# Optimization experiments

Measured on AMD Instinct MI355X. Metric: run time of the kernel, lower is better.

Reference implementation:

```python
import jax, jax.numpy as jnp
import numpy as np

K = 8192  # num_embeddings
D = 512   # embedding_dim
BETA = 0.25


def setup_inputs() -> dict:
    key = jax.random.key(0)
    k1, k2, k3 = jax.random.split(key, 3)
    B, T = 64, 512
    latents = jax.random.normal(k1, (B, T, D), dtype=jnp.float32)
    # nn.Embedding weight initialized uniform(-1/K, 1/K)
    emb = jax.random.uniform(k2, (K, D), dtype=jnp.float32, minval=-1.0 / K, maxval=1.0 / K)
    gold_encoding_inds = jax.random.randint(k3, (B * T, 1), 0, K, dtype=jnp.int64 if jax.config.jax_enable_x64 else jnp.int32)
    return {"gold_encoding_inds": gold_encoding_inds, "latents": latents, "epc": 1, "emb": emb}


def reference(gold_encoding_inds, latents, epc, emb):
    B, T, _ = latents.shape
    flat = latents.reshape(B * T, D)  # [N, D]
    # squared euclidean distance to every codebook entry: [N, K]
    dist = (jnp.sum(flat * flat, axis=1, keepdims=True)
            + jnp.sum(emb * emb, axis=1)
            - 2.0 * jnp.matmul(flat, emb.T))
    encoding_inds = jnp.argmin(dist, axis=1)[:, None]  # [N, 1]
    # one-hot @ emb  ==  gather rows of emb
    quantized = emb[encoding_inds[:, 0]].reshape(B, T, D)
    # per-position MSE over the feature dim
    commitment_loss = jnp.mean((jax.lax.stop_gradient(quantized) - latents) ** 2, axis=-1)
    embedding_loss = jnp.mean((quantized - jax.lax.stop_gradient(latents)) ** 2, axis=-1)
    vq_loss = embedding_loss + BETA * commitment_loss  # [B, T]
    # straight-through estimator
    quantized = latents + jax.lax.stop_gradient(quantized - latents)
    correct = jnp.sum(gold_encoding_inds == encoding_inds)
    total = jnp.asarray(gold_encoding_inds.shape[0], dtype=jnp.int32)
    return quantized, vq_loss, encoding_inds.T, (correct, total)
```

## Files before the change

kernel.cpp:

```cpp
#include <hip/hip_runtime.h>
#include <math.h>

#define N_ROWS 32768
#define KCB    8192
#define DIM    512
#define BETA   0.25f
#define MARGIN 2e-3f
#define FLAG_SLACK 1e-4f
#define CAND_CAP 256

typedef __attribute__((ext_vector_type(4))) float  f32x4;
typedef __attribute__((ext_vector_type(4))) int    i32x4;
typedef __attribute__((ext_vector_type(8))) int    i32x8;

__device__ __forceinline__ unsigned short f2h(float x) {
    _Float16 h = (_Float16)x;
    return *(unsigned short*)&h;
}
__device__ __forceinline__ float h2f(unsigned short u) {
    _Float16 h = *(_Float16*)&u;
    return (float)h;
}

#define SQ_BLOCKS ((N_ROWS + KCB) / 8)
__global__ __launch_bounds__(256) void pre_kernel(
        const float* __restrict__ lat, const float* __restrict__ emb,
        float* __restrict__ row_sq, float* __restrict__ emb_sq,
        unsigned char* __restrict__ latq, unsigned char* __restrict__ embq,
        int* __restrict__ counter) {
    if (blockIdx.x < SQ_BLOCKS) {
#pragma clang fp contract(off)
        if (blockIdx.x == 0 && threadIdx.x == 0) *counter = 0;
        const int w    = threadIdx.x >> 6;
        const int lane = threadIdx.x & 63;
        const int half = lane >> 5;
        const int L    = lane & 31;
        const int b    = L >> 3, j = L & 7;
        const int row  = blockIdx.x * 8 + w * 2 + half;
        const float* p = (row < N_ROWS) ? (lat + (size_t)row * DIM)
                                        : (emb + (size_t)(row - N_ROWS) * DIM);
        const float* q = p + 128 * b + j;
        float a0 = q[0];
        float r  = a0 * a0;
        for (int i = 1; i < 16; ++i) {
            float a = q[8 * i];
            float s = a * a;
            r = r + s;
        }
        r = r + __shfl_xor(r, 1);
        r = r + __shfl_xor(r, 2);
        r = r + __shfl_xor(r, 4);
        r = r + __shfl_xor(r, 8);
        r = r + __shfl_xor(r, 16);
        if (L == 0) {
            if (row < N_ROWS) row_sq[row] = r;
            else              emb_sq[row - N_ROWS] = r;
        }
    } else {
        const size_t NL8 = (size_t)N_ROWS * DIM / 8;
        const size_t NE8 = (size_t)KCB * DIM / 8;
        size_t g = (size_t)(blockIdx.x - SQ_BLOCKS) * 256 + threadIdx.x;
        const float* src; unsigned char* dst; size_t i; float sc;
        if (g < NL8)            { src = lat; dst = latq; i = g;       sc = 1.0f; }
        else if (g < NL8 + NE8) { src = emb; dst = embq; i = g - NL8; sc = 8192.0f; }
        else return;
        float4 v0 = ((const float4*)src)[2 * i];
        float4 v1 = ((const float4*)src)[2 * i + 1];
        int lo = __builtin_amdgcn_cvt_pk_fp8_f32(v0.x * sc, v0.y * sc, 0,  false);
        lo     = __builtin_amdgcn_cvt_pk_fp8_f32(v0.z * sc, v0.w * sc, lo, true);
        int hi = __builtin_amdgcn_cvt_pk_fp8_f32(v1.x * sc, v1.y * sc, 0,  false);
        hi     = __builtin_amdgcn_cvt_pk_fp8_f32(v1.z * sc, v1.w * sc, hi, true);
        ((int2*)dst)[i] = make_int2(lo, hi);
    }
}

__device__ __forceinline__ void load16_to_lds(const void* g, void* l) {
    __builtin_amdgcn_global_load_lds(
        (const __attribute__((address_space(1))) unsigned int*)g,
        (__attribute__((address_space(3))) unsigned int*)l, 16, 0, 0);
}

__global__ __launch_bounds__(256, 2) void gemm_kernel(
        const unsigned char* __restrict__ latq,
        const unsigned char* __restrict__ embq,
        const float* __restrict__ emb_sq,
        unsigned int* __restrict__ packed) {
    __shared__ unsigned char Ac[2][128 * 128];
    __shared__ unsigned char Br[2][128 * 128];

    const int tid   = threadIdx.x;
    const int w     = tid >> 6;
    const int lane  = tid & 63;
    const int q     = lane >> 4;
    const int m16   = lane & 15;

    const int b   = blockIdx.x;
    const int l   = (b & 7) * 2048 + (b >> 3);
    const int st  = l >> 9;
    const int r2  = l & 511;
    const int rg  = st & 7;
    const int cg  = st >> 3;
    const int row0  = (rg * 32 + (r2 & 31)) * 128;
    const int code0 = (cg * 16 + (r2 >> 5)) * 128;

    const int wc    = 64 * (w >> 1);
    const int rbase = 64 * (w & 1);

    int soff[8];
#pragma unroll
    for (int i = 0; i < 8; ++i) {
        int cid   = w * 8 + i;
        int h     = cid & 15;
        int base0 = (cid < 16) ? code0 : row0;
        soff[i] = (base0 + h * 8 + (lane >> 3)) * DIM
                + (((lane & 7) ^ (lane >> 3)) << 4);
    }

#define STAGE(bsel, k0)                                                     \
    do {                                                                    \
        _Pragma("unroll")                                                   \
        for (int i = 0; i < 8; ++i) {                                       \
            int cid = w * 8 + i;                                            \
            const unsigned char* g =                                        \
                ((cid < 16) ? embq : latq) + soff[i] + (k0);                \
            unsigned char* dst = ((cid < 16) ? &Ac[bsel][0] : &Br[bsel][0]) \
                               + (cid & 15) * 1024;                         \
            load16_to_lds(g, dst);                                          \
        }                                                                   \
    } while (0)

    f32x4 acc[4][4];
#pragma unroll
    for (int r = 0; r < 4; ++r)
#pragma unroll
        for (int c = 0; c < 4; ++c) acc[r][c] = (f32x4){0.f, 0.f, 0.f, 0.f};

    const int sw = (m16 & 7) << 4;

    STAGE(0, 0);

#pragma unroll
    for (int t = 0; t < 4; ++t) {
        const int bsel = t & 1;
        if (t < 3) STAGE((t + 1) & 1, (t + 1) * 128);
        __builtin_amdgcn_sched_barrier(0);
        if (t < 3) { asm volatile("s_waitcnt vmcnt(8)" ::: "memory"); }
        else       { asm volatile("s_waitcnt vmcnt(0)" ::: "memory"); }
        __builtin_amdgcn_s_barrier();
        __builtin_amdgcn_sched_barrier(0);

        i32x8 af[4];
#pragma unroll
        for (int r = 0; r < 4; ++r) {
            int roff = (wc + 16 * r + m16) * 128;
            i32x4 lo = *(const i32x4*)&Ac[bsel][roff + ((q * 32) ^ sw)];
            i32x4 hi = *(const i32x4*)&Ac[bsel][roff + ((q * 32 + 16) ^ sw)];
            af[r] = (i32x8){lo[0], lo[1], lo[2], lo[3],
                            hi[0], hi[1], hi[2], hi[3]};
        }
#pragma unroll
        for (int c = 0; c < 4; ++c) {
            int roff = (rbase + 16 * c + m16) * 128;
            i32x4 lo = *(const i32x4*)&Br[bsel][roff + ((q * 32) ^ sw)];
            i32x4 hi = *(const i32x4*)&Br[bsel][roff + ((q * 32 + 16) ^ sw)];
            i32x8 bv = (i32x8){lo[0], lo[1], lo[2], lo[3],
                               hi[0], hi[1], hi[2], hi[3]};
#pragma unroll
            for (int r = 0; r < 4; ++r)
                acc[r][c] = __builtin_amdgcn_mfma_scale_f32_16x16x128_f8f6f4(
                    af[r], bv, acc[r][c],
                    0, 0,
                    0, 0x7F7F7F7F,
                    0, 0x7F7F7F7F);
        }
        __builtin_amdgcn_sched_barrier(0);
        __builtin_amdgcn_s_barrier();
        __builtin_amdgcn_sched_barrier(0);
    }
#undef STAGE

    float sev[4][4];
#pragma unroll
    for (int r = 0; r < 4; ++r)
#pragma unroll
        for (int reg = 0; reg < 4; ++reg)
            sev[r][reg] = emb_sq[code0 + wc + 16 * r + 4 * q + reg];

    const float inv = 1.0f / 4096.0f;
#pragma unroll
    for (int c = 0; c < 4; ++c) {
        unsigned pk[4];
#pragma unroll
        for (int r = 0; r < 4; ++r) {
            float s0 = sev[r][0] - acc[r][c][0] * inv;
            float s1 = sev[r][1] - acc[r][c][1] * inv;
            float s2 = sev[r][2] - acc[r][c][2] * inv;
            float s3 = sev[r][3] - acc[r][c][3] * inv;
            float mn = fminf(fminf(s0, s1), fminf(s2, s3));
            mn = fminf(mn, __shfl_xor(mn, 16));
            mn = fminf(mn, __shfl_xor(mn, 32));
            float t = mn + MARGIN;
            unsigned nib = (s0 <= t ? 1u : 0u) | (s1 <= t ? 2u : 0u)
                         | (s2 <= t ? 4u : 0u) | (s3 <= t ? 8u : 0u);
            nib <<= (4 * q);
            nib |= (unsigned)__shfl_xor((int)nib, 16);
            nib |= (unsigned)__shfl_xor((int)nib, 32);
            pk[r] = ((unsigned)f2h(mn)) | (nib << 16);
        }
        if (lane < 16) {
            int grow = row0 + rbase + 16 * c + m16;
            int base = (code0 + wc) >> 4;
            *(uint4*)&packed[(size_t)grow * 512 + base] =
                make_uint4(pk[0], pk[1], pk[2], pk[3]);
        }
    }
}

__global__ __launch_bounds__(256) void argmin_out_kernel(
        const float* __restrict__ lat, const float* __restrict__ emb,
        const float* __restrict__ row_sq, const float* __restrict__ emb_sq,
        const unsigned int* __restrict__ packed,
        const int* __restrict__ gold,
        float* __restrict__ out, int* __restrict__ counter) {
    __shared__ float xs[4][DIM];
    __shared__ int   s_cnt[4];
    __shared__ int   s_list[4][CAND_CAP];
    const int w    = threadIdx.x >> 6;
    const int lane = threadIdx.x & 63;
    const int row  = blockIdx.x * 4 + w;

    {
        const float4* xp = (const float4*)(lat + (size_t)row * DIM);
        ((float4*)xs[w])[lane]      = xp[lane];
        ((float4*)xs[w])[lane + 64] = xp[lane + 64];
    }
    const float sx = row_sq[row];
    const float* xw = xs[w];

    unsigned u[8];
    {
        const uint4* tb = (const uint4*)(packed + (size_t)row * 512 + lane * 8);
        uint4 v0 = tb[0], v1 = tb[1];
        u[0] = v0.x; u[1] = v0.y; u[2] = v0.z; u[3] = v0.w;
        u[4] = v1.x; u[5] = v1.y; u[6] = v1.z; u[7] = v1.w;
    }
    float tm[8];
#pragma unroll
    for (int j = 0; j < 8; ++j) tm[j] = h2f((unsigned short)(u[j] & 0xFFFFu));
    float m = tm[0];
#pragma unroll
    for (int j = 1; j < 8; ++j) m = fminf(m, tm[j]);
#pragma unroll
    for (int off = 1; off < 64; off <<= 1)
        m = fminf(m, __shfl_xor(m, off));
    const float thresh = m + (MARGIN + FLAG_SLACK);

    if (lane == 0) s_cnt[w] = 0;
    __syncthreads();
#pragma unroll
    for (int j = 0; j < 8; ++j) {
        if (tm[j] <= thresh) {
            int g = lane * 8 + j;
            unsigned bm = u[j] >> 16;
            while (bm) {
                int b = __ffs(bm) - 1;
                bm &= bm - 1;
                int pos = atomicAdd(&s_cnt[w], 1);
                if (pos < CAND_CAP) s_list[w][pos] = g * 16 + b;
            }
        }
    }
    __syncthreads();
    const int cnt = min(s_cnt[w], CAND_CAP);

    float bd = INFINITY;
    int   bi = 0x7fffffff;
    for (int base = 0; base < cnt; base += 64) {
        int ci = base + lane;
        float dvl = INFINITY;
        int   cl  = 0x7fffffff;
        if (ci < cnt) {
            int code = s_list[w][ci];
            const float* ep = emb + (size_t)code * DIM;
            float acc = 0.0f;
            for (int d = 0; d < DIM; d += 8) {
                float ev[8], xv[8];
#pragma unroll
                for (int t = 0; t < 8; ++t) { ev[t] = ep[d + t]; xv[t] = xw[d + t]; }
#pragma unroll
                for (int t = 0; t < 8; ++t) acc = fmaf(xv[t], ev[t], acc);
            }
            float a = sx + emb_sq[code];
            dvl = a - 2.0f * acc;
            cl  = code;
        }
        if (dvl < bd || (dvl == bd && cl < bi)) { bd = dvl; bi = cl; }
    }
#pragma unroll
    for (int off = 1; off < 64; off <<= 1) {
        float od = __shfl_xor(bd, off);
        int   oi = __shfl_xor(bi, off);
        if (od < bd || (od == bd && oi < bi)) { bd = od; bi = oi; }
    }
    const int idx = bi;

    const float4* e4 = (const float4*)(emb + (size_t)idx * DIM);
    float4*       q4 = (float4*)(out + (size_t)row * DIM);
    q4[lane]      = e4[lane];
    q4[lane + 64] = e4[lane + 64];

    float r = 0.0f;
    if (lane < 32) {
        const int b = lane >> 3, j = lane & 7;
        const float* ep = emb + (size_t)idx * DIM + b * 128 + j;
        const float* xp = xw + b * 128 + j;
        for (int i = 0; i < 16; ++i) {
            float dq = ep[8 * i] - xp[8 * i];
            float s  = dq * dq;
            r = (i == 0) ? s : (r + s);
        }
    }
    for (int mm = 1; mm <= 16; mm <<= 1) {
        float o = __shfl_xor(r, mm);
        r = r + o;
    }
    if (lane == 0) {
        float mean = r * (1.0f / 512.0f);
        float v    = mean + 0.25f * mean;
        out[(size_t)N_ROWS * DIM + row]          = v;
        out[(size_t)N_ROWS * DIM + N_ROWS + row] = (float)idx;
        if (gold[row] == idx) atomicAdd(counter, 1);
    }
}

__global__ void tail_kernel(const int* __restrict__ counter,
                            float* __restrict__ out) {
    if (threadIdx.x == 0 && blockIdx.x == 0) {
        const size_t off = (size_t)N_ROWS * DIM + 2 * (size_t)N_ROWS;
        out[off]     = (float)(*counter);
        out[off + 1] = (float)N_ROWS;
    }
}

__global__ __launch_bounds__(256) void sq_kernel(
        const float* __restrict__ lat, const float* __restrict__ emb,
        float* __restrict__ row_sq, float* __restrict__ emb_sq) {
#pragma clang fp contract(off)
    const int w    = threadIdx.x >> 6;
    const int lane = threadIdx.x & 63;
    const int half = lane >> 5;
    const int L    = lane & 31;
    const int b    = L >> 3, j = L & 7;
    const int row  = blockIdx.x * 8 + w * 2 + half;
    if (row >= N_ROWS + KCB) return;
    const float* p = (row < N_ROWS) ? (lat + (size_t)row * DIM)
                                    : (emb + (size_t)(row - N_ROWS) * DIM);
    const float* q = p + 128 * b + j;
    float a0 = q[0];
    float r  = a0 * a0;
    for (int i = 1; i < 16; ++i) {
        float a = q[8 * i];
        float s = a * a;
        r = r + s;
    }
    r = r + __shfl_xor(r, 1);
    r = r + __shfl_xor(r, 2);
    r = r + __shfl_xor(r, 4);
    r = r + __shfl_xor(r, 8);
    r = r + __shfl_xor(r, 16);
    if (L == 0) {
        if (row < N_ROWS) row_sq[row] = r;
        else              emb_sq[row - N_ROWS] = r;
    }
}

#define BM 64
#define BK 128
#define BD 32
__global__ __launch_bounds__(256) void dist_kernel(
        const float* __restrict__ lat, const float* __restrict__ emb,
        const float* __restrict__ row_sq, const float* __restrict__ emb_sq,
        int* __restrict__ enc) {
    __shared__ float xsh[BD][BM];
    __shared__ float esh[BD][BK];
    const int tid  = threadIdx.x;
    const int trow = tid >> 4;
    const int tcol = tid & 15;
    const int row0 = blockIdx.x * BM;
    float bd[4]; int bi[4];
    for (int i = 0; i < 4; ++i) { bd[i] = INFINITY; bi[i] = 0; }
    float sx[4];
    for (int i = 0; i < 4; ++i) sx[i] = row_sq[row0 + 4 * trow + i];
    for (int kt = 0; kt < KCB; kt += BK) {
        float acc[4][8] = {};
        for (int d0 = 0; d0 < DIM; d0 += BD) {
            for (int f = tid; f < BM * BD / 4; f += 256) {
                int r = f >> 3, c4 = f & 7;
                float4 v = *(const float4*)(lat + (size_t)(row0 + r) * DIM + d0 + 4 * c4);
                xsh[4 * c4 + 0][r] = v.x; xsh[4 * c4 + 1][r] = v.y;
                xsh[4 * c4 + 2][r] = v.z; xsh[4 * c4 + 3][r] = v.w;
            }
            for (int f = tid; f < BK * BD / 4; f += 256) {
                int r = f >> 3, c4 = f & 7;
                float4 v = *(const float4*)(emb + (size_t)(kt + r) * DIM + d0 + 4 * c4);
                esh[4 * c4 + 0][r] = v.x; esh[4 * c4 + 1][r] = v.y;
                esh[4 * c4 + 2][r] = v.z; esh[4 * c4 + 3][r] = v.w;
            }
            __syncthreads();
            for (int dd = 0; dd < BD; ++dd) {
                float4 xv  = *(const float4*)&xsh[dd][4 * trow];
                float4 ev0 = *(const float4*)&esh[dd][8 * tcol];
                float4 ev1 = *(const float4*)&esh[dd][8 * tcol + 4];
                float xr[4] = { xv.x, xv.y, xv.z, xv.w };
                float ec[8] = { ev0.x, ev0.y, ev0.z, ev0.w, ev1.x, ev1.y, ev1.z, ev1.w };
                for (int r = 0; r < 4; ++r)
                    for (int c = 0; c < 8; ++c)
                        acc[r][c] = fmaf(xr[r], ec[c], acc[r][c]);
            }
            __syncthreads();
        }
        for (int c = 0; c < 8; ++c) {
            int   code = kt + 8 * tcol + c;
            float se   = emb_sq[code];
            for (int r = 0; r < 4; ++r) {
                float a  = sx[r] + se;
                float dv = a - 2.0f * acc[r][c];
                if (dv < bd[r]) { bd[r] = dv; bi[r] = code; }
            }
        }
    }
    for (int off = 1; off < 16; off <<= 1) {
        for (int r = 0; r < 4; ++r) {
            float od = __shfl_xor(bd[r], off);
            int   oi = __shfl_xor(bi[r], off);
            if (od < bd[r] || (od == bd[r] && oi < bi[r])) { bd[r] = od; bi[r] = oi; }
        }
    }
    if (tcol == 0)
        for (int r = 0; r < 4; ++r)
            enc[row0 + 4 * trow + r] = bi[r];
}

__global__ void out_kernel(const float* __restrict__ lat,
                           const float* __restrict__ emb,
                           const int* __restrict__ gold,
                           const int* __restrict__ enc,
                           float* __restrict__ out,
                           int* __restrict__ counter) {
#pragma clang fp contract(off)
    const int gid  = blockIdx.x * blockDim.x + threadIdx.x;
    const int row  = gid >> 6;
    const int lane = threadIdx.x & 63;
    if (row >= N_ROWS) return;
    const int idx = enc[row];
    const float4* e4 = (const float4*)(emb + (size_t)idx * DIM);
    float4*       q4 = (float4*)(out + (size_t)row * DIM);
    q4[lane]      = e4[lane];
    q4[lane + 64] = e4[lane + 64];
    float r = 0.0f;
    if (lane < 32) {
        const int b = lane >> 3, j = lane & 7;
        const float* ep = emb + (size_t)idx * DIM + b * 128 + j;
        const float* xp = lat + (size_t)row * DIM + b * 128 + j;
        for (int i = 0; i < 16; ++i) {
            float dq = ep[8 * i] - xp[8 * i];
            float s  = dq * dq;
            r = (i == 0) ? s : (r + s);
        }
    }
    for (int m = 1; m <= 16; m <<= 1) {
        float o = __shfl_xor(r, m);
        r = r + o;
    }
    if (lane == 0) {
        float mean = r * (1.0f / 512.0f);
        float v    = mean + 0.25f * mean;
        out[(size_t)N_ROWS * DIM + row]          = v;
        out[(size_t)N_ROWS * DIM + N_ROWS + row] = (float)idx;
        if (gold[row] == idx) atomicAdd(counter, 1);
    }
}

extern "C" void kernel_launch(void* const* d_in, const int* in_sizes, int n_in,
                              void* d_out, int out_size, void* d_ws, size_t ws_size,
                              hipStream_t stream) {
    (void)in_sizes; (void)n_in; (void)out_size;
    const int*   gold = (const int*)d_in[0];
    const float* lat  = (const float*)d_in[1];
    const float* emb  = (const float*)d_in[3];
    float* out = (float*)d_out;

    const size_t SZ_LATQ = (size_t)N_ROWS * DIM;
    const size_t SZ_EMBQ = (size_t)KCB * DIM;
    const size_t SZ_PK   = (size_t)N_ROWS * 512 * 4;
    const size_t SZ_SMALL = (size_t)N_ROWS * 4 + (size_t)KCB * 4 + 256;
    const size_t NEEDED = SZ_LATQ + SZ_EMBQ + SZ_PK + SZ_SMALL;

    if (ws_size >= NEEDED) {
        unsigned char* w8 = (unsigned char*)d_ws;
        unsigned char* latq    = w8;
        unsigned char* embq    = w8 + SZ_LATQ;
        unsigned int*  packed  = (unsigned int*)(w8 + SZ_LATQ + SZ_EMBQ);
        float*         row_sq  = (float*)(w8 + SZ_LATQ + SZ_EMBQ + SZ_PK);
        float*         emb_sq  = row_sq + N_ROWS;
        int*           counter = (int*)(emb_sq + KCB);

        const int pre_blocks = SQ_BLOCKS + (N_ROWS + KCB) * (DIM / 8) / 256;
        pre_kernel<<<pre_blocks, 256, 0, stream>>>(
            lat, emb, row_sq, emb_sq, latq, embq, counter);
        gemm_kernel<<<(N_ROWS / 128) * (KCB / 128), 256, 0, stream>>>(
            latq, embq, emb_sq, packed);
        argmin_out_kernel<<<N_ROWS / 4, 256, 0, stream>>>(
            lat, emb, row_sq, emb_sq, packed, gold, out, counter);
        tail_kernel<<<1, 64, 0, stream>>>(counter, out);
    } else {
        float* row_sq  = (float*)d_ws;
        float* emb_sq  = row_sq + N_ROWS;
        int*   enc     = (int*)(emb_sq + KCB);
        int*   counter = enc + N_ROWS;
        hipMemsetAsync(counter, 0, sizeof(int), stream);
        sq_kernel<<<(N_ROWS + KCB) / 8, 256, 0, stream>>>(lat, emb, row_sq, emb_sq);
        dist_kernel<<<N_ROWS / BM, 256, 0, stream>>>(lat, emb, row_sq, emb_sq, enc);
        out_kernel<<<N_ROWS / 4, 256, 0, stream>>>(lat, emb, gold, enc, out, counter);
        tail_kernel<<<1, 64, 0, stream>>>(counter, out);
    }
}
```

Baseline: 538.8 us.

## Enlarge GEMM tile to 256x256 with 512 threads and XCD-aware block mapping

```diff
diff --git a/kernel.cpp b/kernel.cpp
--- a/kernel.cpp
+++ b/kernel.cpp
@@ -80,38 +80,38 @@
         (__attribute__((address_space(3))) unsigned int*)l, 16, 0, 0);
 }
 
-__global__ __launch_bounds__(256, 2) void gemm_kernel(
+__global__ __launch_bounds__(512, 2) void gemm_kernel(
         const unsigned char* __restrict__ latq,
         const unsigned char* __restrict__ embq,
         const float* __restrict__ emb_sq,
         unsigned int* __restrict__ packed) {
-    __shared__ unsigned char Ac[2][128 * 128];
-    __shared__ unsigned char Br[2][128 * 128];
-
-    const int tid   = threadIdx.x;
-    const int w     = tid >> 6;
-    const int lane  = tid & 63;
-    const int q     = lane >> 4;
-    const int m16   = lane & 15;
+    __shared__ unsigned char Ac[2][256 * 128];
+    __shared__ unsigned char Br[2][256 * 128];
+
+    const int tid  = threadIdx.x;
+    const int w    = tid >> 6;
+    const int lane = tid & 63;
+    const int q    = lane >> 4;
+    const int m16  = lane & 15;
 
     const int b   = blockIdx.x;
-    const int l   = (b & 7) * 2048 + (b >> 3);
-    const int st  = l >> 9;
-    const int r2  = l & 511;
-    const int rg  = st & 7;
-    const int cg  = st >> 3;
-    const int row0  = (rg * 32 + (r2 & 31)) * 128;
-    const int code0 = (cg * 16 + (r2 >> 5)) * 128;
-
-    const int wc    = 64 * (w >> 1);
-    const int rbase = 64 * (w & 1);
+    const int xcd = b & 7;
+    const int id  = b >> 3;
+    const int st  = id >> 6;
+    const int rw  = id & 15;
+    const int cw  = (id >> 4) & 3;
+    const int row0  = (st * 16 + rw) * 256;
+    const int code0 = (xcd * 4 + cw) * 256;
+
+    const int wc2 = (w & 1) * 128;
+    const int wr  = (w >> 1) * 64;
 
     int soff[8];
 #pragma unroll
     for (int i = 0; i < 8; ++i) {
         int cid   = w * 8 + i;
-        int h     = cid & 15;
-        int base0 = (cid < 16) ? code0 : row0;
+        int h     = cid & 31;
+        int base0 = (cid < 32) ? code0 : row0;
         soff[i] = (base0 + h * 8 + (lane >> 3)) * DIM
                 + (((lane & 7) ^ (lane >> 3)) << 4);
     }
@@ -122,18 +122,18 @@
         for (int i = 0; i < 8; ++i) {                                       \
             int cid = w * 8 + i;                                            \
             const unsigned char* g =                                        \
-                ((cid < 16) ? embq : latq) + soff[i] + (k0);                \
-            unsigned char* dst = ((cid < 16) ? &Ac[bsel][0] : &Br[bsel][0]) \
-                               + (cid & 15) * 1024;                         \
+                ((cid < 32) ? embq : latq) + soff[i] + (k0);                \
+            unsigned char* dst = ((cid < 32) ? &Ac[bsel][0] : &Br[bsel][0]) \
+                               + (cid & 31) * 1024;                         \
             load16_to_lds(g, dst);                                          \
         }                                                                   \
     } while (0)
 
-    f32x4 acc[4][4];
-#pragma unroll
-    for (int r = 0; r < 4; ++r)
-#pragma unroll
-        for (int c = 0; c < 4; ++c) acc[r][c] = (f32x4){0.f, 0.f, 0.f, 0.f};
+    f32x4 acc[8][4];
+#pragma unroll
+    for (int g = 0; g < 8; ++g)
+#pragma unroll
+        for (int c = 0; c < 4; ++c) acc[g][c] = (f32x4){0.f, 0.f, 0.f, 0.f};
 
     const int sw = (m16 & 7) << 4;
 
@@ -149,29 +149,38 @@
         __builtin_amdgcn_s_barrier();
         __builtin_amdgcn_sched_barrier(0);
 
-        i32x8 af[4];
-#pragma unroll
-        for (int r = 0; r < 4; ++r) {
-            int roff = (wc + 16 * r + m16) * 128;
-            i32x4 lo = *(const i32x4*)&Ac[bsel][roff + ((q * 32) ^ sw)];
-            i32x4 hi = *(const i32x4*)&Ac[bsel][roff + ((q * 32 + 16) ^ sw)];
-            af[r] = (i32x8){lo[0], lo[1], lo[2], lo[3],
-                            hi[0], hi[1], hi[2], hi[3]};
-        }
+        i32x8 bv[4];
 #pragma unroll
         for (int c = 0; c < 4; ++c) {
-            int roff = (rbase + 16 * c + m16) * 128;
+            int roff = (wr + 16 * c + m16) * 128;
             i32x4 lo = *(const i32x4*)&Br[bsel][roff + ((q * 32) ^ sw)];
             i32x4 hi = *(const i32x4*)&Br[bsel][roff + ((q * 32 + 16) ^ sw)];
-            i32x8 bv = (i32x8){lo[0], lo[1], lo[2], lo[3],
-                               hi[0], hi[1], hi[2], hi[3]};
-#pragma unroll
-            for (int r = 0; r < 4; ++r)
-                acc[r][c] = __builtin_amdgcn_mfma_scale_f32_16x16x128_f8f6f4(
-                    af[r], bv, acc[r][c],
-                    0, 0,
-                    0, 0x7F7F7F7F,
-                    0, 0x7F7F7F7F);
+            bv[c] = (i32x8){lo[0], lo[1], lo[2], lo[3],
+                            hi[0], hi[1], hi[2], hi[3]};
+        }
+#pragma unroll
+        for (int hh = 0; hh < 2; ++hh) {
+            i32x8 af[4];
+#pragma unroll
+            for (int g = 0; g < 4; ++g) {
+                int roff = (wc2 + 16 * (hh * 4 + g) + m16) * 128;
+                i32x4 lo = *(const i32x4*)&Ac[bsel][roff + ((q * 32) ^ sw)];
+                i32x4 hi = *(const i32x4*)&Ac[bsel][roff + ((q * 32 + 16) ^ sw)];
+                af[g] = (i32x8){lo[0], lo[1], lo[2], lo[3],
+                                hi[0], hi[1], hi[2], hi[3]};
+            }
+            __builtin_amdgcn_s_setprio(1);
+#pragma unroll
+            for (int g = 0; g < 4; ++g)
+#pragma unroll
+                for (int c = 0; c < 4; ++c)
+                    acc[hh * 4 + g][c] =
+                        __builtin_amdgcn_mfma_scale_f32_16x16x128_f8f6f4(
+                            af[g], bv[c], acc[hh * 4 + g][c],
+                            0, 0,
+                            0, 0x7F7F7F7F,
+                            0, 0x7F7F7F7F);
+            __builtin_amdgcn_s_setprio(0);
         }
         __builtin_amdgcn_sched_barrier(0);
         __builtin_amdgcn_s_barrier();
@@ -179,23 +188,23 @@
     }
 #undef STAGE
 
-    float sev[4][4];
-#pragma unroll
-    for (int r = 0; r < 4; ++r)
-#pragma unroll
-        for (int reg = 0; reg < 4; ++reg)
-            sev[r][reg] = emb_sq[code0 + wc + 16 * r + 4 * q + reg];
+    float sev[8][4];
+#pragma unroll
+    for (int g = 0; g < 8; ++g)
+#pragma unroll
+        for (int r = 0; r < 4; ++r)
+            sev[g][r] = emb_sq[code0 + wc2 + 16 * g + 4 * q + r];
 
     const float inv = 1.0f / 4096.0f;
 #pragma unroll
     for (int c = 0; c < 4; ++c) {
-        unsigned pk[4];
-#pragma unroll
-        for (int r = 0; r < 4; ++r) {
-            float s0 = sev[r][0] - acc[r][c][0] * inv;
-            float s1 = sev[r][1] - acc[r][c][1] * inv;
-            float s2 = sev[r][2] - acc[r][c][2] * inv;
-            float s3 = sev[r][3] - acc[r][c][3] * inv;
+        unsigned pk[8];
+#pragma unroll
+        for (int g = 0; g < 8; ++g) {
+            float s0 = sev[g][0] - acc[g][c][0] * inv;
+            float s1 = sev[g][1] - acc[g][c][1] * inv;
+            float s2 = sev[g][2] - acc[g][c][2] * inv;
+            float s3 = sev[g][3] - acc[g][c][3] * inv;
             float mn = fminf(fminf(s0, s1), fminf(s2, s3));
             mn = fminf(mn, __shfl_xor(mn, 16));
             mn = fminf(mn, __shfl_xor(mn, 32));
@@ -205,13 +214,15 @@
             nib <<= (4 * q);
             nib |= (unsigned)__shfl_xor((int)nib, 16);
             nib |= (unsigned)__shfl_xor((int)nib, 32);
-            pk[r] = ((unsigned)f2h(mn)) | (nib << 16);
+            pk[g] = ((unsigned)f2h(mn)) | (nib << 16);
         }
         if (lane < 16) {
-            int grow = row0 + rbase + 16 * c + m16;
-            int base = (code0 + wc) >> 4;
+            int grow = row0 + wr + 16 * c + m16;
+            int base = (code0 + wc2) >> 4;
             *(uint4*)&packed[(size_t)grow * 512 + base] =
                 make_uint4(pk[0], pk[1], pk[2], pk[3]);
+            *(uint4*)&packed[(size_t)grow * 512 + base + 4] =
+                make_uint4(pk[4], pk[5], pk[6], pk[7]);
         }
     }
 }
@@ -508,7 +519,7 @@
         const int pre_blocks = SQ_BLOCKS + (N_ROWS + KCB) * (DIM / 8) / 256;
         pre_kernel<<<pre_blocks, 256, 0, stream>>>(
             lat, emb, row_sq, emb_sq, latq, embq, counter);
-        gemm_kernel<<<(N_ROWS / 128) * (KCB / 128), 256, 0, stream>>>(
+        gemm_kernel<<<(N_ROWS / 256) * (KCB / 256), 512, 0, stream>>>(
             latq, embq, emb_sq, packed);
         argmin_out_kernel<<<N_ROWS / 4, 256, 0, stream>>>(
             lat, emb, row_sq, emb_sq, packed, gold, out, counter);
```

After: 715.7 us. +32.8%, slower.
